# Kernel optimization log

Measured on AMD Instinct MI355X. Metric: run time of the kernel, lower is better.

The kernel has to match this reference:

```python
import jax, jax.numpy as jnp
import numpy as np

EPS = 1e-6
MIN_EIG = 1e-4
TAU = 1.0  # obs_temperature


def _expm(A):
    """Batched matrix exponential for small KxK matrices via scaling-and-squaring
    + 12-term Taylor (matches torch.linalg.matrix_exp to ~1e-6 for moderate norms).
    Fully differentiable in both modes. A: (..., K, K)."""
    s = 6
    A = A * (1.0 / 2.0 ** s)
    I = jnp.eye(A.shape[-1], dtype=A.dtype)
    E = I + A
    term = A
    for k in range(2, 13):
        term = jnp.matmul(term, A) / k
        E = E + term
    for _ in range(s):
        E = jnp.matmul(E, E)
    return E


def setup_inputs() -> dict:
    key = jax.random.key(0)
    ks = jax.random.split(key, 6)
    B, N, K, V = 1, 2048, 3, 8192
    I = jnp.eye(K, dtype=jnp.float32)
    Ap = jax.random.normal(ks[0], (B, N, K, K), jnp.float32)
    Sigma_prior = Ap @ jnp.swapaxes(Ap, -1, -2) / K + 0.5 * I  # SPD
    Aq = jax.random.normal(ks[1], (B, N, K, K), jnp.float32)
    Sigma_q = Aq @ jnp.swapaxes(Aq, -1, -2) / K + 0.5 * I  # SPD
    phi = 0.5 * jax.random.normal(ks[2], (B, N, 3), jnp.float32)
    beta = jax.nn.softmax(jax.random.normal(ks[3], (B, N, N), jnp.float32), axis=-1)
    mu = jax.random.normal(ks[4], (B, N, K), jnp.float32)
    W_out = jax.random.normal(ks[5], (V, K), jnp.float32) / jnp.sqrt(float(K))
    generators = jnp.array([[[0, 0, 0], [0, 0, -1], [0, 1, 0]],
                            [[0, 0, 1], [0, 0, 0], [-1, 0, 0]],
                            [[0, -1, 0], [1, 0, 0], [0, 0, 0]]], jnp.float32)
    return dict(Sigma_prior=Sigma_prior, Sigma_q=Sigma_q, phi=phi, beta=beta,
                mu=mu, W_out=W_out, generators=generators)


def reference(Sigma_prior, Sigma_q, phi, beta, mu, W_out, generators):
    B, N, K = mu.shape
    dt = Sigma_prior.dtype
    I = jnp.eye(K, dtype=dt)

    # Prior precision Lambda_p = (Sigma_p + eps I)^{-1}
    Lambda_p = jnp.linalg.inv(Sigma_prior + EPS * I)

    # Categorical observation precision: Lambda_o = Cov_p(W) / tau^2
    logits = jnp.einsum('bnk,vk->bnv', mu, W_out) / TAU
    p = jax.nn.softmax(logits, axis=-1)                                # (B,N,V)
    mean_w = jnp.einsum('bnv,vk->bnk', p, W_out)                        # E_p[w]
    second = jnp.einsum('bnv,vk,vl->bnkl', p, W_out, W_out)             # E_p[ww^T]
    Lambda_o = (second - jnp.einsum('bnk,bnl->bnkl', mean_w, mean_w)) / TAU ** 2
    Lambda_o = 0.5 * (Lambda_o + jnp.swapaxes(Lambda_o, -1, -2)) + EPS * I

    # Posterior precision
    Lambda_q = jnp.linalg.inv(Sigma_q + EPS * I)                        # (B,N,K,K)

    # Gauge transport Omega_{ij} = e^{phi_i} e^{-phi_j}
    phi_mat = jnp.einsum('bnc,ckl->bnkl', phi, generators)              # (B,N,K,K)
    exp_phi = _expm(phi_mat)
    exp_neg_phi = _expm(-phi_mat)
    Omega = jnp.einsum('bikl,bjlm->bijkm', exp_phi, exp_neg_phi)        # (B,N,N,K,K)

    # Transported precision Lambda~_{qj in i-frame} = Omega Lambda_q Omega^T
    Lt = jnp.einsum('bijkl,bjlm,bijnm->bijkn', Omega, Lambda_q, Omega)  # (B,N,N,K,K)
    M_incoming = jnp.einsum('bij,bijkn->bikn', beta, Lt)                # (B,N,K,K)

    # Outgoing recoil: (sum_j beta_{ji}) * Lambda_{qi}
    M_outgoing = beta.sum(axis=1)[..., None, None] * Lambda_q

    M = Lambda_p + Lambda_o + M_incoming + M_outgoing
    M = 0.5 * (M + jnp.swapaxes(M, -1, -2))
    bad = ~jnp.isfinite(M)
    M = jnp.where(bad, jnp.broadcast_to(I, M.shape), M)
    M = M + max(MIN_EIG, 1e-4) * I

    # Eigenvalue floor and inverse
    w, v = jnp.linalg.eigh(M.astype(jnp.float32))
    w = jnp.clip(w, MIN_EIG, None)
    M_pd = jnp.einsum('...ij,...j,...kj->...ik', v, w, v)
    M_inv = jnp.einsum('...ij,...j,...kj->...ik', v, 1.0 / w, v)
    return M_pd.astype(dt), M_inv.astype(dt)
```

## Files before the change

kernel.cpp:

```cpp
#include <hip/hip_runtime.h>
#include <math.h>

#define EPSV 1e-6f
#define MINEIG 1e-4f


__device__ __forceinline__ void mm3(const float a[3][3], const float b[3][3], float c[3][3]) {
#pragma unroll
  for (int i = 0; i < 3; ++i)
#pragma unroll
    for (int j = 0; j < 3; ++j)
      c[i][j] = fmaf(a[i][0], b[0][j], fmaf(a[i][1], b[1][j], a[i][2] * b[2][j]));
}

__device__ __forceinline__ void inv3(const float a[3][3], float inv[3][3]) {
  float c00 = a[1][1] * a[2][2] - a[1][2] * a[2][1];
  float c01 = -(a[1][0] * a[2][2] - a[1][2] * a[2][0]);
  float c02 = a[1][0] * a[2][1] - a[1][1] * a[2][0];
  float det = a[0][0] * c00 + a[0][1] * c01 + a[0][2] * c02;
  float id = 1.0f / det;
  inv[0][0] = c00 * id;
  inv[0][1] = (a[0][2] * a[2][1] - a[0][1] * a[2][2]) * id;
  inv[0][2] = (a[0][1] * a[1][2] - a[0][2] * a[1][1]) * id;
  inv[1][0] = c01 * id;
  inv[1][1] = (a[0][0] * a[2][2] - a[0][2] * a[2][0]) * id;
  inv[1][2] = (a[0][2] * a[1][0] - a[0][0] * a[1][2]) * id;
  inv[2][0] = c02 * id;
  inv[2][1] = (a[0][1] * a[2][0] - a[0][0] * a[2][1]) * id;
  inv[2][2] = (a[0][0] * a[1][1] - a[0][1] * a[1][0]) * id;
}

__device__ void expm3(const float A[3][3], float E[3][3]) {
  float As[3][3], term[3][3], tmp[3][3];
#pragma unroll
  for (int i = 0; i < 3; ++i)
#pragma unroll
    for (int j = 0; j < 3; ++j) {
      As[i][j] = A[i][j] * (1.0f / 64.0f);
      term[i][j] = As[i][j];
      E[i][j] = ((i == j) ? 1.0f : 0.0f) + As[i][j];
    }
  for (int k = 2; k <= 12; ++k) {
    mm3(term, As, tmp);
    float r = 1.0f / (float)k;
#pragma unroll
    for (int i = 0; i < 3; ++i)
#pragma unroll
      for (int j = 0; j < 3; ++j) {
        term[i][j] = tmp[i][j] * r;
        E[i][j] += term[i][j];
      }
  }
  for (int s = 0; s < 6; ++s) {
    mm3(E, E, tmp);
#pragma unroll
    for (int i = 0; i < 3; ++i)
#pragma unroll
      for (int j = 0; j < 3; ++j) E[i][j] = tmp[i][j];
  }
}

template <int P, int Q, int RI>
__device__ __forceinline__ void jrot(float A[3][3], float V[3][3]) {
  float apq = A[P][Q];
  if (fabsf(apq) < 1e-20f) return;
  float theta = (A[Q][Q] - A[P][P]) / (2.0f * apq);
  float t = copysignf(1.0f, theta) / (fabsf(theta) + sqrtf(fmaf(theta, theta, 1.0f)));
  float c = 1.0f / sqrtf(fmaf(t, t, 1.0f));
  float s = t * c;
  A[P][P] = A[P][P] - t * apq;
  A[Q][Q] = A[Q][Q] + t * apq;
  A[P][Q] = 0.f; A[Q][P] = 0.f;
  float arp = A[RI][P], arq = A[RI][Q];
  float nrp = c * arp - s * arq;
  float nrq = s * arp + c * arq;
  A[RI][P] = nrp; A[P][RI] = nrp;
  A[RI][Q] = nrq; A[Q][RI] = nrq;
#pragma unroll
  for (int i = 0; i < 3; ++i) {
    float vip = V[i][P], viq = V[i][Q];
    V[i][P] = c * vip - s * viq;
    V[i][Q] = s * vip + c * viq;
  }
}

__device__ __forceinline__ bool finitef(float x) {
  return !(isnan(x) || isinf(x));
}


__global__ void prep_colsum_kernel(const float* __restrict__ Sp, const float* __restrict__ Sq,
                                   const float* __restrict__ phi, const float* __restrict__ gen,
                                   const float* __restrict__ beta,
                                   float* __restrict__ Lp, float* __restrict__ Lq,
                                   float* __restrict__ Rm, float* __restrict__ Ssoa,
                                   float* __restrict__ pcs, int N) {
  int bid = blockIdx.x;
  int tid = threadIdx.x;
  int nPrep = N >> 8;
  if (bid < nPrep) {
    int i = bid * 256 + tid;
    float a[3][3], lp[3][3], lq[3][3];
#pragma unroll
    for (int k = 0; k < 3; ++k)
#pragma unroll
      for (int l = 0; l < 3; ++l)
        a[k][l] = Sp[i * 9 + k * 3 + l] + ((k == l) ? EPSV : 0.0f);
    inv3(a, lp);
#pragma unroll
    for (int k = 0; k < 3; ++k)
#pragma unroll
      for (int l = 0; l < 3; ++l)
        a[k][l] = Sq[i * 9 + k * 3 + l] + ((k == l) ? EPSV : 0.0f);
    inv3(a, lq);

    float p0 = phi[i * 3 + 0], p1 = phi[i * 3 + 1], p2 = phi[i * 3 + 2];
    float A[3][3];
#pragma unroll
    for (int k = 0; k < 3; ++k)
#pragma unroll
      for (int l = 0; l < 3; ++l)
        A[k][l] = p0 * gen[0 + k * 3 + l] + p1 * gen[9 + k * 3 + l] + p2 * gen[18 + k * 3 + l];
    float R[3][3];
    expm3(A, R);
    float Rt[3][3];
#pragma unroll
    for (int k = 0; k < 3; ++k)
#pragma unroll
      for (int l = 0; l < 3; ++l) Rt[k][l] = R[l][k];
    float t1[3][3], S[3][3];
    mm3(lq, R, t1);
    mm3(Rt, t1, S);
#pragma unroll
    for (int k = 0; k < 3; ++k)
#pragma unroll
      for (int l = 0; l < 3; ++l) {
        Lp[i * 9 + k * 3 + l] = lp[k][l];
        Lq[i * 9 + k * 3 + l] = lq[k][l];
        Rm[i * 9 + k * 3 + l] = R[k][l];
        Ssoa[(k * 3 + l) * N + i] = S[k][l];
      }
  } else {
    int cb = bid - nPrep;
    int nCT = N >> 8;
    int rs = cb / nCT;
    int ct = cb % nCT;
    int j = ct * 256 + tid;
    const float* bp = beta + (size_t)(rs * 32) * N + j;
    float s = 0.f;
#pragma unroll
    for (int r = 0; r < 32; ++r) s += bp[(size_t)r * N];
    pcs[(size_t)rs * N + j] = s;
  }
}


__global__ void bmm_kernel(const float* __restrict__ beta, const float* __restrict__ Ssoa,
                           float* __restrict__ T, int N) {
  int lane = threadIdx.x & 63;
  int w = threadIdx.x >> 6;
  int i = blockIdx.x * 4 + w;
  const float4* B4 = (const float4*)(beta + (size_t)i * N);
  float acc[9];
#pragma unroll
  for (int k = 0; k < 9; ++k) acc[k] = 0.f;

  for (int jt = 0; jt < N; jt += 256) {
    int q = (jt >> 2) + lane;
    float4 b = B4[q];
    float4 sv[9];
#pragma unroll
    for (int k = 0; k < 9; ++k) sv[k] = ((const float4*)(Ssoa + k * N))[q];
#pragma unroll
    for (int k = 0; k < 9; ++k) {
      acc[k] = fmaf(b.x, sv[k].x, acc[k]);
      acc[k] = fmaf(b.y, sv[k].y, acc[k]);
      acc[k] = fmaf(b.z, sv[k].z, acc[k]);
      acc[k] = fmaf(b.w, sv[k].w, acc[k]);
    }
  }
#pragma unroll
  for (int k = 0; k < 9; ++k) {
    float x = acc[k];
#pragma unroll
    for (int o = 32; o > 0; o >>= 1) x += __shfl_down(x, o, 64);
    if (lane == 0) T[i * 9 + k] = x;
  }
}


__global__ void lo_kernel(const float* __restrict__ mu, const float* __restrict__ W,
                          float* __restrict__ Lo, int V) {
  int n0 = blockIdx.x * 4;
  int tid = threadIdx.x;
  float m[4][3];
#pragma unroll
  for (int j = 0; j < 4; ++j) {
    m[j][0] = mu[(n0 + j) * 3 + 0];
    m[j][1] = mu[(n0 + j) * 3 + 1];
    m[j][2] = mu[(n0 + j) * 3 + 2];
  }
  float acc[4][10];
#pragma unroll
  for (int j = 0; j < 4; ++j)
#pragma unroll
    for (int k = 0; k < 10; ++k) acc[j][k] = 0.f;

  const float4* W4 = (const float4*)W;
  for (int vb = tid; vb * 4 < V; vb += 256) {
    float4 f0 = W4[vb * 3 + 0];
    float4 f1 = W4[vb * 3 + 1];
    float4 f2 = W4[vb * 3 + 2];
    float wv[4][3] = {{f0.x, f0.y, f0.z}, {f0.w, f1.x, f1.y},
                      {f1.z, f1.w, f2.x}, {f2.y, f2.z, f2.w}};
#pragma unroll
    for (int c = 0; c < 4; ++c) {
      float w0 = wv[c][0], w1 = wv[c][1], w2 = wv[c][2];
      float p00 = w0 * w0, p01 = w0 * w1, p02 = w0 * w2;
      float p11 = w1 * w1, p12 = w1 * w2, p22 = w2 * w2;
#pragma unroll
      for (int j = 0; j < 4; ++j) {
        float l = fmaf(m[j][0], w0, fmaf(m[j][1], w1, m[j][2] * w2));
        float e = __expf(l);
        acc[j][0] += e;
        acc[j][1] = fmaf(e, w0, acc[j][1]);
        acc[j][2] = fmaf(e, w1, acc[j][2]);
        acc[j][3] = fmaf(e, w2, acc[j][3]);
        acc[j][4] = fmaf(e, p00, acc[j][4]);
        acc[j][5] = fmaf(e, p01, acc[j][5]);
        acc[j][6] = fmaf(e, p02, acc[j][6]);
        acc[j][7] = fmaf(e, p11, acc[j][7]);
        acc[j][8] = fmaf(e, p12, acc[j][8]);
        acc[j][9] = fmaf(e, p22, acc[j][9]);
      }
    }
  }

  __shared__ float sred[4][40];
#pragma unroll
  for (int j = 0; j < 4; ++j)
#pragma unroll
    for (int k = 0; k < 10; ++k) {
      float x = acc[j][k];
#pragma unroll
      for (int o = 32; o > 0; o >>= 1) x += __shfl_down(x, o, 64);
      if ((tid & 63) == 0) sred[tid >> 6][j * 10 + k] = x;
    }
  __syncthreads();
  if (tid < 4) {
    int j = tid;
    float tot[10];
#pragma unroll
    for (int k = 0; k < 10; ++k)
      tot[k] = sred[0][j * 10 + k] + sred[1][j * 10 + k] +
               sred[2][j * 10 + k] + sred[3][j * 10 + k];
    float inv = 1.0f / tot[0];
    float mw0 = tot[1] * inv, mw1 = tot[2] * inv, mw2 = tot[3] * inv;
    float* o = Lo + (n0 + j) * 9;
    o[0] = tot[4] * inv - mw0 * mw0 + EPSV;
    float v01 = tot[5] * inv - mw0 * mw1;
    float v02 = tot[6] * inv - mw0 * mw2;
    o[1] = v01; o[3] = v01;
    o[2] = v02; o[6] = v02;
    o[4] = tot[7] * inv - mw1 * mw1 + EPSV;
    float v12 = tot[8] * inv - mw1 * mw2;
    o[5] = v12; o[7] = v12;
    o[8] = tot[9] * inv - mw2 * mw2 + EPSV;
  }
}


__global__ void finalize_kernel(const float* __restrict__ Lp, const float* __restrict__ Lq,
                                const float* __restrict__ Rm, const float* __restrict__ Lo,
                                const float* __restrict__ T, const float* __restrict__ pcs,
                                float* __restrict__ out, int N) {
  int i = blockIdx.x * blockDim.x + threadIdx.x;
  if (i >= N) return;

  float c = 0.f;
  int RS = N >> 5;
  for (int r = 0; r < RS; ++r) c += pcs[(size_t)r * N + i];

  float R[3][3], Tm[3][3], M[3][3];
#pragma unroll
  for (int k = 0; k < 3; ++k)
#pragma unroll
    for (int l = 0; l < 3; ++l) {
      R[k][l] = Rm[i * 9 + k * 3 + l];
      Tm[k][l] = T[i * 9 + k * 3 + l];
    }
  float t1[3][3], Rt[3][3], Min[3][3];
  mm3(R, Tm, t1);
#pragma unroll
  for (int k = 0; k < 3; ++k)
#pragma unroll
    for (int l = 0; l < 3; ++l) Rt[k][l] = R[l][k];
  mm3(t1, Rt, Min);
#pragma unroll
  for (int k = 0; k < 3; ++k)
#pragma unroll
    for (int l = 0; l < 3; ++l)
      M[k][l] = Lp[i * 9 + k * 3 + l] + Lo[i * 9 + k * 3 + l] + Min[k][l] +
                c * Lq[i * 9 + k * 3 + l];
#pragma unroll
  for (int k = 0; k < 3; ++k)
#pragma unroll
    for (int l = 0; l < 3; ++l) {
      if (l > k) {
        float v = 0.5f * (M[k][l] + M[l][k]);
        M[k][l] = v; M[l][k] = v;
      }
    }
#pragma unroll
  for (int k = 0; k < 3; ++k)
#pragma unroll
    for (int l = 0; l < 3; ++l)
      if (!finitef(M[k][l])) M[k][l] = (k == l) ? 1.0f : 0.0f;
  M[0][0] += MINEIG; M[1][1] += MINEIG; M[2][2] += MINEIG;

  float A[3][3], Vv[3][3] = {{1, 0, 0}, {0, 1, 0}, {0, 0, 1}};
#pragma unroll
  for (int k = 0; k < 3; ++k)
#pragma unroll
    for (int l = 0; l < 3; ++l) A[k][l] = M[k][l];
  for (int sweep = 0; sweep < 8; ++sweep) {
    jrot<0, 1, 2>(A, Vv);
    jrot<0, 2, 1>(A, Vv);
    jrot<1, 2, 0>(A, Vv);
  }
  float wc[3], wi[3];
#pragma unroll
  for (int k = 0; k < 3; ++k) {
    wc[k] = fmaxf(A[k][k], MINEIG);
    wi[k] = 1.0f / wc[k];
  }
#pragma unroll
  for (int k = 0; k < 3; ++k)
#pragma unroll
    for (int l = 0; l < 3; ++l) {
      float mpd = Vv[k][0] * wc[0] * Vv[l][0] + Vv[k][1] * wc[1] * Vv[l][1] +
                  Vv[k][2] * wc[2] * Vv[l][2];
      float mnv = Vv[k][0] * wi[0] * Vv[l][0] + Vv[k][1] * wi[1] * Vv[l][1] +
                  Vv[k][2] * wi[2] * Vv[l][2];
      out[i * 9 + k * 3 + l] = mpd;
      out[(size_t)N * 9 + i * 9 + k * 3 + l] = mnv;
    }
}


extern "C" void kernel_launch(void* const* d_in, const int* in_sizes, int n_in,
                              void* d_out, int out_size, void* d_ws, size_t ws_size,
                              hipStream_t stream) {
  const float* Sp = (const float*)d_in[0];
  const float* Sq = (const float*)d_in[1];
  const float* phi = (const float*)d_in[2];
  const float* beta = (const float*)d_in[3];
  const float* mu = (const float*)d_in[4];
  const float* W = (const float*)d_in[5];
  const float* gen = (const float*)d_in[6];
  float* out = (float*)d_out;

  const int N = in_sizes[2] / 3;
  const int V = in_sizes[5] / 3;

  float* ws = (float*)d_ws;
  float* Lp = ws;
  float* Lq = Lp + (size_t)N * 9;
  float* Rm = Lq + (size_t)N * 9;
  float* Ssoa = Rm + (size_t)N * 9;
  float* T = Ssoa + (size_t)N * 9;
  float* Lo = T + (size_t)N * 9;
  float* pcs = Lo + (size_t)N * 9;

  int nPrep = N / 256;
  int nColsum = (N / 32) * (N / 256);
  prep_colsum_kernel<<<nPrep + nColsum, 256, 0, stream>>>(Sp, Sq, phi, gen, beta,
                                                          Lp, Lq, Rm, Ssoa, pcs, N);
  lo_kernel<<<N / 4, 256, 0, stream>>>(mu, W, Lo, V);
  bmm_kernel<<<N / 4, 256, 0, stream>>>(beta, Ssoa, T, N);
  finalize_kernel<<<N / 256, 256, 0, stream>>>(Lp, Lq, Rm, Lo, T, pcs, out, N);
}
```

Measured before the change: 126.0 us.

## Fuse four kernels into two stages and register-block beta rows in bmm

The Lo softmax-moment computation moves into the prep/colsum launch as extra blocks, so independent work shares one launch. The beta-by-S batched product is fused with the finalize step: each wave now handles four rows, reusing the loaded S vectors across them, and runs the eigen-decomposition finalize in-wave without writing T to memory. This removes two launches and the T round trip. In exchange, stageC has only N/16 blocks with heavily redundant per-lane Jacobi work, which lowers parallelism for the finalize step.

After: 131.3 us. +4.2%, slower.

```diff
diff --git a/kernel.cpp b/kernel.cpp
--- a/kernel.cpp
+++ b/kernel.cpp
@@ -89,15 +89,18 @@
 }
 
 
-__global__ void prep_colsum_kernel(const float* __restrict__ Sp, const float* __restrict__ Sq,
-                                   const float* __restrict__ phi, const float* __restrict__ gen,
-                                   const float* __restrict__ beta,
-                                   float* __restrict__ Lp, float* __restrict__ Lq,
-                                   float* __restrict__ Rm, float* __restrict__ Ssoa,
-                                   float* __restrict__ pcs, int N) {
+__global__ void stageA_kernel(const float* __restrict__ Sp, const float* __restrict__ Sq,
+                              const float* __restrict__ phi, const float* __restrict__ gen,
+                              const float* __restrict__ beta, const float* __restrict__ mu,
+                              const float* __restrict__ W,
+                              float* __restrict__ Lp, float* __restrict__ Lq,
+                              float* __restrict__ Rm, float* __restrict__ Ssoa,
+                              float* __restrict__ pcs, float* __restrict__ Lo,
+                              int N, int V) {
   int bid = blockIdx.x;
   int tid = threadIdx.x;
   int nPrep = N >> 8;
+  int nColsum = (N >> 5) * (N >> 8);
   if (bid < nPrep) {
     int i = bid * 256 + tid;
     float a[3][3], lp[3][3], lq[3][3];
@@ -140,7 +143,7 @@
         Rm[i * 9 + k * 3 + l] = R[k][l];
         Ssoa[(k * 3 + l) * N + i] = S[k][l];
       }
-  } else {
+  } else if (bid < nPrep + nColsum) {
     int cb = bid - nPrep;
     int nCT = N >> 8;
     int rs = cb / nCT;
@@ -151,200 +154,208 @@
 #pragma unroll
     for (int r = 0; r < 32; ++r) s += bp[(size_t)r * N];
     pcs[(size_t)rs * N + j] = s;
-  }
-}
-
-
-__global__ void bmm_kernel(const float* __restrict__ beta, const float* __restrict__ Ssoa,
-                           float* __restrict__ T, int N) {
+  } else {
+    int n0 = (bid - nPrep - nColsum) * 4;
+    float m[4][3];
+#pragma unroll
+    for (int j = 0; j < 4; ++j) {
+      m[j][0] = mu[(n0 + j) * 3 + 0];
+      m[j][1] = mu[(n0 + j) * 3 + 1];
+      m[j][2] = mu[(n0 + j) * 3 + 2];
+    }
+    float acc[4][10];
+#pragma unroll
+    for (int j = 0; j < 4; ++j)
+#pragma unroll
+      for (int k = 0; k < 10; ++k) acc[j][k] = 0.f;
+
+    const float4* W4 = (const float4*)W;
+    for (int vb = tid; vb * 4 < V; vb += 256) {
+      float4 f0 = W4[vb * 3 + 0];
+      float4 f1 = W4[vb * 3 + 1];
+      float4 f2 = W4[vb * 3 + 2];
+      float wv[4][3] = {{f0.x, f0.y, f0.z}, {f0.w, f1.x, f1.y},
+                        {f1.z, f1.w, f2.x}, {f2.y, f2.z, f2.w}};
+#pragma unroll
+      for (int c = 0; c < 4; ++c) {
+        float w0 = wv[c][0], w1 = wv[c][1], w2 = wv[c][2];
+        float p00 = w0 * w0, p01 = w0 * w1, p02 = w0 * w2;
+        float p11 = w1 * w1, p12 = w1 * w2, p22 = w2 * w2;
+#pragma unroll
+        for (int j = 0; j < 4; ++j) {
+          float l = fmaf(m[j][0], w0, fmaf(m[j][1], w1, m[j][2] * w2));
+          float e = __expf(l);
+          acc[j][0] += e;
+          acc[j][1] = fmaf(e, w0, acc[j][1]);
+          acc[j][2] = fmaf(e, w1, acc[j][2]);
+          acc[j][3] = fmaf(e, w2, acc[j][3]);
+          acc[j][4] = fmaf(e, p00, acc[j][4]);
+          acc[j][5] = fmaf(e, p01, acc[j][5]);
+          acc[j][6] = fmaf(e, p02, acc[j][6]);
+          acc[j][7] = fmaf(e, p11, acc[j][7]);
+          acc[j][8] = fmaf(e, p12, acc[j][8]);
+          acc[j][9] = fmaf(e, p22, acc[j][9]);
+        }
+      }
+    }
+
+    __shared__ float sred[4][40];
+#pragma unroll
+    for (int j = 0; j < 4; ++j)
+#pragma unroll
+      for (int k = 0; k < 10; ++k) {
+        float x = acc[j][k];
+#pragma unroll
+        for (int o = 32; o > 0; o >>= 1) x += __shfl_down(x, o, 64);
+        if ((tid & 63) == 0) sred[tid >> 6][j * 10 + k] = x;
+      }
+    __syncthreads();
+    if (tid < 4) {
+      int j = tid;
+      float tot[10];
+#pragma unroll
+      for (int k = 0; k < 10; ++k)
+        tot[k] = sred[0][j * 10 + k] + sred[1][j * 10 + k] +
+                 sred[2][j * 10 + k] + sred[3][j * 10 + k];
+      float inv = 1.0f / tot[0];
+      float mw0 = tot[1] * inv, mw1 = tot[2] * inv, mw2 = tot[3] * inv;
+      float* o = Lo + (n0 + j) * 9;
+      o[0] = tot[4] * inv - mw0 * mw0 + EPSV;
+      float v01 = tot[5] * inv - mw0 * mw1;
+      float v02 = tot[6] * inv - mw0 * mw2;
+      o[1] = v01; o[3] = v01;
+      o[2] = v02; o[6] = v02;
+      o[4] = tot[7] * inv - mw1 * mw1 + EPSV;
+      float v12 = tot[8] * inv - mw1 * mw2;
+      o[5] = v12; o[7] = v12;
+      o[8] = tot[9] * inv - mw2 * mw2 + EPSV;
+    }
+  }
+}
+
+
+__global__ void stageC_kernel(const float* __restrict__ beta, const float* __restrict__ Ssoa,
+                              const float* __restrict__ Lp, const float* __restrict__ Lq,
+                              const float* __restrict__ Rm, const float* __restrict__ Lo,
+                              const float* __restrict__ pcs, float* __restrict__ out,
+                              int N) {
   int lane = threadIdx.x & 63;
   int w = threadIdx.x >> 6;
-  int i = blockIdx.x * 4 + w;
-  const float4* B4 = (const float4*)(beta + (size_t)i * N);
-  float acc[9];
-#pragma unroll
-  for (int k = 0; k < 9; ++k) acc[k] = 0.f;
+  int i0 = blockIdx.x * 16 + w * 4;
+
+  float acc[4][9];
+#pragma unroll
+  for (int r = 0; r < 4; ++r)
+#pragma unroll
+    for (int k = 0; k < 9; ++k) acc[r][k] = 0.f;
+
+  const float4* B4[4];
+#pragma unroll
+  for (int r = 0; r < 4; ++r) B4[r] = (const float4*)(beta + (size_t)(i0 + r) * N);
 
   for (int jt = 0; jt < N; jt += 256) {
     int q = (jt >> 2) + lane;
-    float4 b = B4[q];
     float4 sv[9];
 #pragma unroll
     for (int k = 0; k < 9; ++k) sv[k] = ((const float4*)(Ssoa + k * N))[q];
 #pragma unroll
+    for (int r = 0; r < 4; ++r) {
+      float4 b = B4[r][q];
+#pragma unroll
+      for (int k = 0; k < 9; ++k) {
+        acc[r][k] = fmaf(b.x, sv[k].x, acc[r][k]);
+        acc[r][k] = fmaf(b.y, sv[k].y, acc[r][k]);
+        acc[r][k] = fmaf(b.z, sv[k].z, acc[r][k]);
+        acc[r][k] = fmaf(b.w, sv[k].w, acc[r][k]);
+      }
+    }
+  }
+
+  int RS = N >> 5;
+#pragma unroll
+  for (int r = 0; r < 4; ++r) {
+    int i = i0 + r;
+    float tv[9];
+#pragma unroll
     for (int k = 0; k < 9; ++k) {
-      acc[k] = fmaf(b.x, sv[k].x, acc[k]);
-      acc[k] = fmaf(b.y, sv[k].y, acc[k]);
-      acc[k] = fmaf(b.z, sv[k].z, acc[k]);
-      acc[k] = fmaf(b.w, sv[k].w, acc[k]);
-    }
-  }
-#pragma unroll
-  for (int k = 0; k < 9; ++k) {
-    float x = acc[k];
-#pragma unroll
-    for (int o = 32; o > 0; o >>= 1) x += __shfl_down(x, o, 64);
-    if (lane == 0) T[i * 9 + k] = x;
-  }
-}
-
-
-__global__ void lo_kernel(const float* __restrict__ mu, const float* __restrict__ W,
-                          float* __restrict__ Lo, int V) {
-  int n0 = blockIdx.x * 4;
-  int tid = threadIdx.x;
-  float m[4][3];
-#pragma unroll
-  for (int j = 0; j < 4; ++j) {
-    m[j][0] = mu[(n0 + j) * 3 + 0];
-    m[j][1] = mu[(n0 + j) * 3 + 1];
-    m[j][2] = mu[(n0 + j) * 3 + 2];
-  }
-  float acc[4][10];
-#pragma unroll
-  for (int j = 0; j < 4; ++j)
-#pragma unroll
-    for (int k = 0; k < 10; ++k) acc[j][k] = 0.f;
-
-  const float4* W4 = (const float4*)W;
-  for (int vb = tid; vb * 4 < V; vb += 256) {
-    float4 f0 = W4[vb * 3 + 0];
-    float4 f1 = W4[vb * 3 + 1];
-    float4 f2 = W4[vb * 3 + 2];
-    float wv[4][3] = {{f0.x, f0.y, f0.z}, {f0.w, f1.x, f1.y},
-                      {f1.z, f1.w, f2.x}, {f2.y, f2.z, f2.w}};
-#pragma unroll
-    for (int c = 0; c < 4; ++c) {
-      float w0 = wv[c][0], w1 = wv[c][1], w2 = wv[c][2];
-      float p00 = w0 * w0, p01 = w0 * w1, p02 = w0 * w2;
-      float p11 = w1 * w1, p12 = w1 * w2, p22 = w2 * w2;
-#pragma unroll
-      for (int j = 0; j < 4; ++j) {
-        float l = fmaf(m[j][0], w0, fmaf(m[j][1], w1, m[j][2] * w2));
-        float e = __expf(l);
-        acc[j][0] += e;
-        acc[j][1] = fmaf(e, w0, acc[j][1]);
-        acc[j][2] = fmaf(e, w1, acc[j][2]);
-        acc[j][3] = fmaf(e, w2, acc[j][3]);
-        acc[j][4] = fmaf(e, p00, acc[j][4]);
-        acc[j][5] = fmaf(e, p01, acc[j][5]);
-        acc[j][6] = fmaf(e, p02, acc[j][6]);
-        acc[j][7] = fmaf(e, p11, acc[j][7]);
-        acc[j][8] = fmaf(e, p12, acc[j][8]);
-        acc[j][9] = fmaf(e, p22, acc[j][9]);
-      }
-    }
-  }
-
-  __shared__ float sred[4][40];
-#pragma unroll
-  for (int j = 0; j < 4; ++j)
-#pragma unroll
-    for (int k = 0; k < 10; ++k) {
-      float x = acc[j][k];
+      float x = acc[r][k];
 #pragma unroll
       for (int o = 32; o > 0; o >>= 1) x += __shfl_down(x, o, 64);
-      if ((tid & 63) == 0) sred[tid >> 6][j * 10 + k] = x;
-    }
-  __syncthreads();
-  if (tid < 4) {
-    int j = tid;
-    float tot[10];
-#pragma unroll
-    for (int k = 0; k < 10; ++k)
-      tot[k] = sred[0][j * 10 + k] + sred[1][j * 10 + k] +
-               sred[2][j * 10 + k] + sred[3][j * 10 + k];
-    float inv = 1.0f / tot[0];
-    float mw0 = tot[1] * inv, mw1 = tot[2] * inv, mw2 = tot[3] * inv;
-    float* o = Lo + (n0 + j) * 9;
-    o[0] = tot[4] * inv - mw0 * mw0 + EPSV;
-    float v01 = tot[5] * inv - mw0 * mw1;
-    float v02 = tot[6] * inv - mw0 * mw2;
-    o[1] = v01; o[3] = v01;
-    o[2] = v02; o[6] = v02;
-    o[4] = tot[7] * inv - mw1 * mw1 + EPSV;
-    float v12 = tot[8] * inv - mw1 * mw2;
-    o[5] = v12; o[7] = v12;
-    o[8] = tot[9] * inv - mw2 * mw2 + EPSV;
-  }
-}
-
-
-__global__ void finalize_kernel(const float* __restrict__ Lp, const float* __restrict__ Lq,
-                                const float* __restrict__ Rm, const float* __restrict__ Lo,
-                                const float* __restrict__ T, const float* __restrict__ pcs,
-                                float* __restrict__ out, int N) {
-  int i = blockIdx.x * blockDim.x + threadIdx.x;
-  if (i >= N) return;
-
-  float c = 0.f;
-  int RS = N >> 5;
-  for (int r = 0; r < RS; ++r) c += pcs[(size_t)r * N + i];
-
-  float R[3][3], Tm[3][3], M[3][3];
-#pragma unroll
-  for (int k = 0; k < 3; ++k)
-#pragma unroll
-    for (int l = 0; l < 3; ++l) {
-      R[k][l] = Rm[i * 9 + k * 3 + l];
-      Tm[k][l] = T[i * 9 + k * 3 + l];
-    }
-  float t1[3][3], Rt[3][3], Min[3][3];
-  mm3(R, Tm, t1);
-#pragma unroll
-  for (int k = 0; k < 3; ++k)
-#pragma unroll
-    for (int l = 0; l < 3; ++l) Rt[k][l] = R[l][k];
-  mm3(t1, Rt, Min);
-#pragma unroll
-  for (int k = 0; k < 3; ++k)
-#pragma unroll
-    for (int l = 0; l < 3; ++l)
-      M[k][l] = Lp[i * 9 + k * 3 + l] + Lo[i * 9 + k * 3 + l] + Min[k][l] +
-                c * Lq[i * 9 + k * 3 + l];
-#pragma unroll
-  for (int k = 0; k < 3; ++k)
-#pragma unroll
-    for (int l = 0; l < 3; ++l) {
-      if (l > k) {
-        float v = 0.5f * (M[k][l] + M[l][k]);
-        M[k][l] = v; M[l][k] = v;
-      }
-    }
-#pragma unroll
-  for (int k = 0; k < 3; ++k)
-#pragma unroll
-    for (int l = 0; l < 3; ++l)
-      if (!finitef(M[k][l])) M[k][l] = (k == l) ? 1.0f : 0.0f;
-  M[0][0] += MINEIG; M[1][1] += MINEIG; M[2][2] += MINEIG;
-
-  float A[3][3], Vv[3][3] = {{1, 0, 0}, {0, 1, 0}, {0, 0, 1}};
-#pragma unroll
-  for (int k = 0; k < 3; ++k)
-#pragma unroll
-    for (int l = 0; l < 3; ++l) A[k][l] = M[k][l];
-  for (int sweep = 0; sweep < 8; ++sweep) {
-    jrot<0, 1, 2>(A, Vv);
-    jrot<0, 2, 1>(A, Vv);
-    jrot<1, 2, 0>(A, Vv);
-  }
-  float wc[3], wi[3];
-#pragma unroll
-  for (int k = 0; k < 3; ++k) {
-    wc[k] = fmaxf(A[k][k], MINEIG);
-    wi[k] = 1.0f / wc[k];
-  }
-#pragma unroll
-  for (int k = 0; k < 3; ++k)
-#pragma unroll
-    for (int l = 0; l < 3; ++l) {
-      float mpd = Vv[k][0] * wc[0] * Vv[l][0] + Vv[k][1] * wc[1] * Vv[l][1] +
-                  Vv[k][2] * wc[2] * Vv[l][2];
-      float mnv = Vv[k][0] * wi[0] * Vv[l][0] + Vv[k][1] * wi[1] * Vv[l][1] +
-                  Vv[k][2] * wi[2] * Vv[l][2];
-      out[i * 9 + k * 3 + l] = mpd;
-      out[(size_t)N * 9 + i * 9 + k * 3 + l] = mnv;
-    }
+      tv[k] = __shfl(x, 0, 64);
+    }
+    float cc = 0.f;
+    for (int rr = lane; rr < RS; rr += 64) cc += pcs[(size_t)rr * N + i];
+#pragma unroll
+    for (int o = 32; o > 0; o >>= 1) cc += __shfl_down(cc, o, 64);
+    float c = __shfl(cc, 0, 64);
+
+    float R[3][3], Tm[3][3], M[3][3];
+#pragma unroll
+    for (int k = 0; k < 3; ++k)
+#pragma unroll
+      for (int l = 0; l < 3; ++l) {
+        R[k][l] = Rm[i * 9 + k * 3 + l];
+        Tm[k][l] = tv[k * 3 + l];
+      }
+    float t1[3][3], Rt[3][3], Min[3][3];
+    mm3(R, Tm, t1);
+#pragma unroll
+    for (int k = 0; k < 3; ++k)
+#pragma unroll
+      for (int l = 0; l < 3; ++l) Rt[k][l] = R[l][k];
+    mm3(t1, Rt, Min);
+#pragma unroll
+    for (int k = 0; k < 3; ++k)
+#pragma unroll
+      for (int l = 0; l < 3; ++l)
+        M[k][l] = Lp[i * 9 + k * 3 + l] + Lo[i * 9 + k * 3 + l] + Min[k][l] +
+                  c * Lq[i * 9 + k * 3 + l];
+#pragma unroll
+    for (int k = 0; k < 3; ++k)
+#pragma unroll
+      for (int l = 0; l < 3; ++l) {
+        if (l > k) {
+          float v = 0.5f * (M[k][l] + M[l][k]);
+          M[k][l] = v; M[l][k] = v;
+        }
+      }
+#pragma unroll
+    for (int k = 0; k < 3; ++k)
+#pragma unroll
+      for (int l = 0; l < 3; ++l)
+        if (!finitef(M[k][l])) M[k][l] = (k == l) ? 1.0f : 0.0f;
+    M[0][0] += MINEIG; M[1][1] += MINEIG; M[2][2] += MINEIG;
+
+    float A[3][3], Vv[3][3] = {{1, 0, 0}, {0, 1, 0}, {0, 0, 1}};
+#pragma unroll
+    for (int k = 0; k < 3; ++k)
+#pragma unroll
+      for (int l = 0; l < 3; ++l) A[k][l] = M[k][l];
+    for (int sweep = 0; sweep < 8; ++sweep) {
+      jrot<0, 1, 2>(A, Vv);
+      jrot<0, 2, 1>(A, Vv);
+      jrot<1, 2, 0>(A, Vv);
+    }
+    float wc[3], wi[3];
+#pragma unroll
+    for (int k = 0; k < 3; ++k) {
+      wc[k] = fmaxf(A[k][k], MINEIG);
+      wi[k] = 1.0f / wc[k];
+    }
+    if (lane == 0) {
+#pragma unroll
+      for (int k = 0; k < 3; ++k)
+#pragma unroll
+        for (int l = 0; l < 3; ++l) {
+          float mpd = Vv[k][0] * wc[0] * Vv[l][0] + Vv[k][1] * wc[1] * Vv[l][1] +
+                      Vv[k][2] * wc[2] * Vv[l][2];
+          float mnv = Vv[k][0] * wi[0] * Vv[l][0] + Vv[k][1] * wi[1] * Vv[l][1] +
+                      Vv[k][2] * wi[2] * Vv[l][2];
+          out[i * 9 + k * 3 + l] = mpd;
+          out[(size_t)N * 9 + i * 9 + k * 3 + l] = mnv;
+        }
+    }
+  }
 }
 
 
@@ -368,15 +379,13 @@
   float* Lq = Lp + (size_t)N * 9;
   float* Rm = Lq + (size_t)N * 9;
   float* Ssoa = Rm + (size_t)N * 9;
-  float* T = Ssoa + (size_t)N * 9;
-  float* Lo = T + (size_t)N * 9;
+  float* Lo = Ssoa + (size_t)N * 9;
   float* pcs = Lo + (size_t)N * 9;
 
   int nPrep = N / 256;
   int nColsum = (N / 32) * (N / 256);
-  prep_colsum_kernel<<<nPrep + nColsum, 256, 0, stream>>>(Sp, Sq, phi, gen, beta,
-                                                          Lp, Lq, Rm, Ssoa, pcs, N);
-  lo_kernel<<<N / 4, 256, 0, stream>>>(mu, W, Lo, V);
-  bmm_kernel<<<N / 4, 256, 0, stream>>>(beta, Ssoa, T, N);
-  finalize_kernel<<<N / 256, 256, 0, stream>>>(Lp, Lq, Rm, Lo, T, pcs, out, N);
-}
+  int nLo = N / 4;
+  stageA_kernel<<<nPrep + nColsum + nLo, 256, 0, stream>>>(
+      Sp, Sq, phi, gen, beta, mu, W, Lp, Lq, Rm, Ssoa, pcs, Lo, N, V);
+  stageC_kernel<<<N / 16, 256, 0, stream>>>(beta, Ssoa, Lp, Lq, Rm, Lo, pcs, out, N);
+}
```

## Fuse observation-precision kernel into prep/colsum launch and vectorize column sums

Applied to the files above, without the earlier changes.

Merges the softmax-covariance (Lo) computation into the same launch as the prep and beta column-sum blocks, so the independent stages run concurrently and one launch is removed. The column-sum blocks now use float4 loads over 8 rows each, which produces more partial rows that the finalize kernel must reduce serially. Workspace order is rearranged to match.

Result: slower. 170.3 us (+35.1%).

```diff
diff --git a/kernel.cpp b/kernel.cpp
--- a/kernel.cpp
+++ b/kernel.cpp
@@ -89,15 +89,19 @@
 }
 
 
-__global__ void prep_colsum_kernel(const float* __restrict__ Sp, const float* __restrict__ Sq,
-                                   const float* __restrict__ phi, const float* __restrict__ gen,
-                                   const float* __restrict__ beta,
-                                   float* __restrict__ Lp, float* __restrict__ Lq,
-                                   float* __restrict__ Rm, float* __restrict__ Ssoa,
-                                   float* __restrict__ pcs, int N) {
+__global__ void stageA_kernel(const float* __restrict__ Sp, const float* __restrict__ Sq,
+                              const float* __restrict__ phi, const float* __restrict__ gen,
+                              const float* __restrict__ beta, const float* __restrict__ mu,
+                              const float* __restrict__ W,
+                              float* __restrict__ Lp, float* __restrict__ Lq,
+                              float* __restrict__ Rm, float* __restrict__ Ssoa,
+                              float* __restrict__ pcs, float* __restrict__ Lo,
+                              int N, int V) {
   int bid = blockIdx.x;
   int tid = threadIdx.x;
   int nPrep = N >> 8;
+  int nCT = N >> 10;
+  int nColsum = (N >> 3) * nCT;
   if (bid < nPrep) {
     int i = bid * 256 + tid;
     float a[3][3], lp[3][3], lq[3][3];
@@ -140,17 +144,95 @@
         Rm[i * 9 + k * 3 + l] = R[k][l];
         Ssoa[(k * 3 + l) * N + i] = S[k][l];
       }
-  } else {
+  } else if (bid < nPrep + nColsum) {
     int cb = bid - nPrep;
-    int nCT = N >> 8;
     int rs = cb / nCT;
     int ct = cb % nCT;
-    int j = ct * 256 + tid;
-    const float* bp = beta + (size_t)(rs * 32) * N + j;
-    float s = 0.f;
-#pragma unroll
-    for (int r = 0; r < 32; ++r) s += bp[(size_t)r * N];
-    pcs[(size_t)rs * N + j] = s;
+    int j4 = ct * 256 + tid;
+    const float4* bp = (const float4*)(beta + (size_t)(rs * 8) * N) + j4;
+    float4 s = {0.f, 0.f, 0.f, 0.f};
+#pragma unroll
+    for (int r = 0; r < 8; ++r) {
+      float4 b = bp[(size_t)r * (N >> 2)];
+      s.x += b.x; s.y += b.y; s.z += b.z; s.w += b.w;
+    }
+    ((float4*)(pcs + (size_t)rs * N))[j4] = s;
+  } else {
+    int n0 = (bid - nPrep - nColsum) * 4;
+    float m[4][3];
+#pragma unroll
+    for (int j = 0; j < 4; ++j) {
+      m[j][0] = mu[(n0 + j) * 3 + 0];
+      m[j][1] = mu[(n0 + j) * 3 + 1];
+      m[j][2] = mu[(n0 + j) * 3 + 2];
+    }
+    float acc[4][10];
+#pragma unroll
+    for (int j = 0; j < 4; ++j)
+#pragma unroll
+      for (int k = 0; k < 10; ++k) acc[j][k] = 0.f;
+
+    const float4* W4 = (const float4*)W;
+    for (int vb = tid; vb * 4 < V; vb += 256) {
+      float4 f0 = W4[vb * 3 + 0];
+      float4 f1 = W4[vb * 3 + 1];
+      float4 f2 = W4[vb * 3 + 2];
+      float wv[4][3] = {{f0.x, f0.y, f0.z}, {f0.w, f1.x, f1.y},
+                        {f1.z, f1.w, f2.x}, {f2.y, f2.z, f2.w}};
+#pragma unroll
+      for (int c = 0; c < 4; ++c) {
+        float w0 = wv[c][0], w1 = wv[c][1], w2 = wv[c][2];
+        float p00 = w0 * w0, p01 = w0 * w1, p02 = w0 * w2;
+        float p11 = w1 * w1, p12 = w1 * w2, p22 = w2 * w2;
+#pragma unroll
+        for (int j = 0; j < 4; ++j) {
+          float l = fmaf(m[j][0], w0, fmaf(m[j][1], w1, m[j][2] * w2));
+          float e = __expf(l);
+          acc[j][0] += e;
+          acc[j][1] = fmaf(e, w0, acc[j][1]);
+          acc[j][2] = fmaf(e, w1, acc[j][2]);
+          acc[j][3] = fmaf(e, w2, acc[j][3]);
+          acc[j][4] = fmaf(e, p00, acc[j][4]);
+          acc[j][5] = fmaf(e, p01, acc[j][5]);
+          acc[j][6] = fmaf(e, p02, acc[j][6]);
+          acc[j][7] = fmaf(e, p11, acc[j][7]);
+          acc[j][8] = fmaf(e, p12, acc[j][8]);
+          acc[j][9] = fmaf(e, p22, acc[j][9]);
+        }
+      }
+    }
+
+    __shared__ float sred[4][40];
+#pragma unroll
+    for (int j = 0; j < 4; ++j)
+#pragma unroll
+      for (int k = 0; k < 10; ++k) {
+        float x = acc[j][k];
+#pragma unroll
+        for (int o = 32; o > 0; o >>= 1) x += __shfl_down(x, o, 64);
+        if ((tid & 63) == 0) sred[tid >> 6][j * 10 + k] = x;
+      }
+    __syncthreads();
+    if (tid < 4) {
+      int j = tid;
+      float tot[10];
+#pragma unroll
+      for (int k = 0; k < 10; ++k)
+        tot[k] = sred[0][j * 10 + k] + sred[1][j * 10 + k] +
+                 sred[2][j * 10 + k] + sred[3][j * 10 + k];
+      float inv = 1.0f / tot[0];
+      float mw0 = tot[1] * inv, mw1 = tot[2] * inv, mw2 = tot[3] * inv;
+      float* o = Lo + (n0 + j) * 9;
+      o[0] = tot[4] * inv - mw0 * mw0 + EPSV;
+      float v01 = tot[5] * inv - mw0 * mw1;
+      float v02 = tot[6] * inv - mw0 * mw2;
+      o[1] = v01; o[3] = v01;
+      o[2] = v02; o[6] = v02;
+      o[4] = tot[7] * inv - mw1 * mw1 + EPSV;
+      float v12 = tot[8] * inv - mw1 * mw2;
+      o[5] = v12; o[7] = v12;
+      o[8] = tot[9] * inv - mw2 * mw2 + EPSV;
+    }
   }
 }
 
@@ -189,87 +271,6 @@
 }
 
 
-__global__ void lo_kernel(const float* __restrict__ mu, const float* __restrict__ W,
-                          float* __restrict__ Lo, int V) {
-  int n0 = blockIdx.x * 4;
-  int tid = threadIdx.x;
-  float m[4][3];
-#pragma unroll
-  for (int j = 0; j < 4; ++j) {
-    m[j][0] = mu[(n0 + j) * 3 + 0];
-    m[j][1] = mu[(n0 + j) * 3 + 1];
-    m[j][2] = mu[(n0 + j) * 3 + 2];
-  }
-  float acc[4][10];
-#pragma unroll
-  for (int j = 0; j < 4; ++j)
-#pragma unroll
-    for (int k = 0; k < 10; ++k) acc[j][k] = 0.f;
-
-  const float4* W4 = (const float4*)W;
-  for (int vb = tid; vb * 4 < V; vb += 256) {
-    float4 f0 = W4[vb * 3 + 0];
-    float4 f1 = W4[vb * 3 + 1];
-    float4 f2 = W4[vb * 3 + 2];
-    float wv[4][3] = {{f0.x, f0.y, f0.z}, {f0.w, f1.x, f1.y},
-                      {f1.z, f1.w, f2.x}, {f2.y, f2.z, f2.w}};
-#pragma unroll
-    for (int c = 0; c < 4; ++c) {
-      float w0 = wv[c][0], w1 = wv[c][1], w2 = wv[c][2];
-      float p00 = w0 * w0, p01 = w0 * w1, p02 = w0 * w2;
-      float p11 = w1 * w1, p12 = w1 * w2, p22 = w2 * w2;
-#pragma unroll
-      for (int j = 0; j < 4; ++j) {
-        float l = fmaf(m[j][0], w0, fmaf(m[j][1], w1, m[j][2] * w2));
-        float e = __expf(l);
-        acc[j][0] += e;
-        acc[j][1] = fmaf(e, w0, acc[j][1]);
-        acc[j][2] = fmaf(e, w1, acc[j][2]);
-        acc[j][3] = fmaf(e, w2, acc[j][3]);
-        acc[j][4] = fmaf(e, p00, acc[j][4]);
-        acc[j][5] = fmaf(e, p01, acc[j][5]);
-        acc[j][6] = fmaf(e, p02, acc[j][6]);
-        acc[j][7] = fmaf(e, p11, acc[j][7]);
-        acc[j][8] = fmaf(e, p12, acc[j][8]);
-        acc[j][9] = fmaf(e, p22, acc[j][9]);
-      }
-    }
-  }
-
-  __shared__ float sred[4][40];
-#pragma unroll
-  for (int j = 0; j < 4; ++j)
-#pragma unroll
-    for (int k = 0; k < 10; ++k) {
-      float x = acc[j][k];
-#pragma unroll
-      for (int o = 32; o > 0; o >>= 1) x += __shfl_down(x, o, 64);
-      if ((tid & 63) == 0) sred[tid >> 6][j * 10 + k] = x;
-    }
-  __syncthreads();
-  if (tid < 4) {
-    int j = tid;
-    float tot[10];
-#pragma unroll
-    for (int k = 0; k < 10; ++k)
-      tot[k] = sred[0][j * 10 + k] + sred[1][j * 10 + k] +
-               sred[2][j * 10 + k] + sred[3][j * 10 + k];
-    float inv = 1.0f / tot[0];
-    float mw0 = tot[1] * inv, mw1 = tot[2] * inv, mw2 = tot[3] * inv;
-    float* o = Lo + (n0 + j) * 9;
-    o[0] = tot[4] * inv - mw0 * mw0 + EPSV;
-    float v01 = tot[5] * inv - mw0 * mw1;
-    float v02 = tot[6] * inv - mw0 * mw2;
-    o[1] = v01; o[3] = v01;
-    o[2] = v02; o[6] = v02;
-    o[4] = tot[7] * inv - mw1 * mw1 + EPSV;
-    float v12 = tot[8] * inv - mw1 * mw2;
-    o[5] = v12; o[7] = v12;
-    o[8] = tot[9] * inv - mw2 * mw2 + EPSV;
-  }
-}
-
-
 __global__ void finalize_kernel(const float* __restrict__ Lp, const float* __restrict__ Lq,
                                 const float* __restrict__ Rm, const float* __restrict__ Lo,
                                 const float* __restrict__ T, const float* __restrict__ pcs,
@@ -278,7 +279,7 @@
   if (i >= N) return;
 
   float c = 0.f;
-  int RS = N >> 5;
+  int RS = N >> 3;
   for (int r = 0; r < RS; ++r) c += pcs[(size_t)r * N + i];
 
   float R[3][3], Tm[3][3], M[3][3];
@@ -368,15 +369,15 @@
   float* Lq = Lp + (size_t)N * 9;
   float* Rm = Lq + (size_t)N * 9;
   float* Ssoa = Rm + (size_t)N * 9;
-  float* T = Ssoa + (size_t)N * 9;
-  float* Lo = T + (size_t)N * 9;
-  float* pcs = Lo + (size_t)N * 9;
+  float* Lo = Ssoa + (size_t)N * 9;
+  float* T = Lo + (size_t)N * 9;
+  float* pcs = T + (size_t)N * 9;
 
   int nPrep = N / 256;
-  int nColsum = (N / 32) * (N / 256);
-  prep_colsum_kernel<<<nPrep + nColsum, 256, 0, stream>>>(Sp, Sq, phi, gen, beta,
-                                                          Lp, Lq, Rm, Ssoa, pcs, N);
-  lo_kernel<<<N / 4, 256, 0, stream>>>(mu, W, Lo, V);
+  int nColsum = (N / 8) * (N / 1024);
+  int nLo = N / 4;
+  stageA_kernel<<<nPrep + nColsum + nLo, 256, 0, stream>>>(
+      Sp, Sq, phi, gen, beta, mu, W, Lp, Lq, Rm, Ssoa, pcs, Lo, N, V);
   bmm_kernel<<<N / 4, 256, 0, stream>>>(beta, Ssoa, T, N);
   finalize_kernel<<<N / 256, 256, 0, stream>>>(Lp, Lq, Rm, Lo, T, pcs, out, N);
 }
```
